# Kernel optimization log

Hardware: AMD Instinct MI355X
Metric: run time of the kernel (lower is better)

The kernel has to match this reference:

```python
import jax, jax.numpy as jnp
import numpy as np

E, DM, DH, K, DIL = 8, 512, 1024, 3, 2
N, L = 128, 128
PAD = DIL * (K - 1) // 2  # 'same' padding


def _conv1d(x, w):
    # x: [N, Cin, L], w: [Cout, Cin, K] -> [N, Cout, L]
    return jax.lax.conv_general_dilated(
        x, w, window_strides=(1,), padding=[(PAD, PAD)],
        rhs_dilation=(DIL,), dimension_numbers=("NCH", "OIH", "NCH"))


def _moe_conv(x, W, B, onehot):
    # W: [E, Cout, Cin, K], B: [E, Cout], onehot: [N, E]
    ys = jax.vmap(lambda w, b: _conv1d(x, w) + b[None, :, None])(W, B)  # [E, N, Cout, L]
    return jnp.einsum("enol,ne->nol", ys, onehot)


def setup_inputs() -> dict:
    key = jax.random.key(0)
    k1, k2, k3, k4, k5 = jax.random.split(key, 5)
    inp = jax.random.normal(k1, (N, DM, L), dtype=jnp.float32)
    # uneven per-expert sample counts summing to N (samples pre-sorted by expert)
    fwd_expert_count = jnp.asarray(np.array([10, 20, 16, 16, 12, 22, 14, 18], dtype=np.int32))
    w1 = jax.random.normal(k2, (E, DH, DM, K), dtype=jnp.float32) * 0.02
    b1 = jax.random.normal(k3, (E, DH), dtype=jnp.float32) * 0.02
    w2 = jax.random.normal(k4, (E, DM, DH, K), dtype=jnp.float32) * 0.02
    b2 = jax.random.normal(k5, (E, DM), dtype=jnp.float32) * 0.02
    return {"inp": inp, "fwd_expert_count": fwd_expert_count,
            "w1": w1, "b1": b1, "w2": w2, "b2": b2}


def reference(inp, fwd_expert_count, w1, b1, w2, b2):
    # map each sample index to its expert via cumulative counts
    cs = jnp.cumsum(fwd_expert_count)
    eid = jnp.searchsorted(cs, jnp.arange(N), side="right")  # [N]
    onehot = (eid[:, None] == jnp.arange(E)[None, :]).astype(inp.dtype)  # [N, E]
    h = _moe_conv(inp, w1, b1, onehot)       # [N, DH, L]
    h = jax.nn.gelu(h)
    out = _moe_conv(h, w2, b2, onehot)       # [N, DM, L]
    return out
```

## Files before the change

### kernel.cpp

```cpp
#include <hip/hip_runtime.h>
#include <hip/hip_bf16.h>
#include <stdint.h>


typedef __attribute__((ext_vector_type(8))) short short8;
typedef __attribute__((ext_vector_type(4))) float f32x4;

#define DMV 512
#define DHV 1024

#define OFF_X   0ull
#define OFF_H   (16ull << 20)
#define OFF_W1  (48ull << 20)
#define OFF_W2  (72ull << 20)

#define VMW(n) asm volatile("s_waitcnt vmcnt(" #n ")" ::: "memory")

__device__ __forceinline__ uint16_t f2bf(float f) {
  uint32_t u = __builtin_bit_cast(uint32_t, f);
  uint32_t r = (u + 0x7FFFu + ((u >> 16) & 1u)) >> 16;
  return (uint16_t)r;
}

__device__ __forceinline__ void async_copy16(const void* g, void* l) {
  __builtin_amdgcn_global_load_lds(
      (const __attribute__((address_space(1))) uint32_t*)g,
      (__attribute__((address_space(3))) uint32_t*)l, 16, 0, 0);
}

__device__ __forceinline__ float gelu_f(float x) {
  float u = 0.7978845608028654f * (x + 0.044715f * x * x * x);
  float t = __expf(2.0f * u);
  float th = 1.0f - 2.0f / (t + 1.0f);
  return 0.5f * x * (1.0f + th);
}

__global__ __launch_bounds__(256) void prep_x_t(const float* __restrict__ inp,
                                                uint16_t* __restrict__ xp) {
  uint32_t b = blockIdx.x;
  uint32_t s = b >> 4, cc = b & 15u;
  __shared__ uint16_t xs[32][132];
  uint32_t t = threadIdx.x;
  const float* src0 = inp + ((size_t)s * DMV + cc * 32u) * 128u;
#pragma unroll
  for (int i = 0; i < 4; ++i) {
    uint32_t idx = (uint32_t)i * 256u + t;
    uint32_t ch = idx >> 5, l4 = idx & 31u;
    float4 f = *(const float4*)(src0 + ch * 128u + l4 * 4u);
    uint2 pk;
    pk.x = (uint32_t)f2bf(f.x) | ((uint32_t)f2bf(f.y) << 16);
    pk.y = (uint32_t)f2bf(f.z) | ((uint32_t)f2bf(f.w) << 16);
    *(uint2*)&xs[ch][l4 * 4u] = pk;
  }
  __syncthreads();
  uint32_t l = t >> 1, half = t & 1u;
  uint32_t fl = ((l + 2u) >> 1) & 3u;
#pragma unroll
  for (int hi = 0; hi < 2; ++hi) {
    uint32_t sub = half * 2u + (uint32_t)hi;
    uint32_t cg = (sub ^ fl) & 3u;
    uint32_t pk[4];
#pragma unroll
    for (int p2 = 0; p2 < 4; ++p2) {
      uint32_t c0 = cg * 8u + (uint32_t)p2 * 2u;
      pk[p2] = (uint32_t)xs[c0][l] | ((uint32_t)xs[c0 + 1][l] << 16);
    }
    uint4 v; v.x = pk[0]; v.y = pk[1]; v.z = pk[2]; v.w = pk[3];
    size_t slot = (((size_t)s * 16u + cc) * 128u + l) * 4u + sub;
    *(uint4*)(xp + slot * 8u) = v;
  }
}

template <int LOGCG, int LOGO>
__global__ __launch_bounds__(256) void prep_w_c(const float* __restrict__ w,
                                                uint16_t* __restrict__ wp) {
  constexpr uint32_t C = 4u << LOGCG;
  constexpr uint32_t CCn = C >> 5;
  constexpr uint32_t MTn = 1u << (LOGO - 7);
  uint32_t t = blockIdx.x * 256u + threadIdx.x;
  uint32_t cg = t & ((1u << LOGCG) - 1u);
  uint32_t o = (t >> LOGCG) & ((1u << LOGO) - 1u);
  uint32_t e = t >> (LOGCG + LOGO);
  uint32_t row = o & 127u, mt = o >> 7;
  const float* src = w + (((size_t)(e << LOGO) + o) * C + cg * 4u) * 3u;
  float4 f0 = *(const float4*)(src);
  float4 f1 = *(const float4*)(src + 4);
  float4 f2 = *(const float4*)(src + 8);
  uint32_t cc = cg >> 3;
  uint32_t sub = ((cg >> 1) & 3u) ^ ((row >> 1) & 3u);
  uint32_t j0 = (cg & 1u) * 4u;
  size_t base = (((size_t)e * CCn + cc) * MTn + mt) * 3u;
  uint2 q;
  q.x = (uint32_t)f2bf(f0.x) | ((uint32_t)f2bf(f0.w) << 16);
  q.y = (uint32_t)f2bf(f1.z) | ((uint32_t)f2bf(f2.y) << 16);
  *(uint2*)(wp + ((base + 0u) * 128u + row) * 32u + sub * 8u + j0) = q;
  q.x = (uint32_t)f2bf(f0.y) | ((uint32_t)f2bf(f1.x) << 16);
  q.y = (uint32_t)f2bf(f1.w) | ((uint32_t)f2bf(f2.z) << 16);
  *(uint2*)(wp + ((base + 1u) * 128u + row) * 32u + sub * 8u + j0) = q;
  q.x = (uint32_t)f2bf(f0.z) | ((uint32_t)f2bf(f1.y) << 16);
  q.y = (uint32_t)f2bf(f2.x) | ((uint32_t)f2bf(f2.w) << 16);
  *(uint2*)(wp + ((base + 2u) * 128u + row) * 32u + sub * 8u + j0) = q;
}

template <int PHASE>
__global__ __launch_bounds__(256, 2) void conv_mfma(
    const uint16_t* __restrict__ bprep, const uint16_t* __restrict__ wprep,
    const float* __restrict__ bias, const int* __restrict__ cnt,
    uint16_t* __restrict__ hout, float* __restrict__ fout) {
  constexpr int CC = (PHASE == 1) ? 16 : 32;
  constexpr int MTP = (PHASE == 1) ? 8 : 4;
  constexpr int OO = (PHASE == 1) ? DHV : DMV;
  constexpr uint32_t BUFS = 24576u + 8448u;

  uint32_t b = blockIdx.x;
  constexpr uint32_t CPX = (128u * MTP) >> 3;
  uint32_t work = (b & 7u) * CPX + (b >> 3);
  const int s = work & 127;
  const int mt = work >> 7;
  int e = 0;
  {
    int cum = cnt[0];
    while (s >= cum && e < 7) { ++e; cum += cnt[e]; }
  }
  const int tid = threadIdx.x;
  const int lane = tid & 63;
  const int wv = tid >> 6;
  const int wr = wv >> 1, wc = wv & 1;
  const int l15 = lane & 15, kg = lane >> 4;

  __shared__ __align__(16) uint8_t lds[2 * BUFS];

  uint32_t aOff[4];
#pragma unroll
  for (int a = 0; a < 4; ++a) {
    uint32_t ri = (uint32_t)(wr * 64 + a * 16 + l15);
    aOff[a] = ri * 64u + (((uint32_t)kg ^ (ri >> 1)) & 3u) * 16u;
  }
  uint32_t lB[4];
#pragma unroll
  for (int bq = 0; bq < 4; ++bq) lB[bq] = (uint32_t)(wc * 64 + bq * 16 + l15);

  const uint16_t* wTile0 = wprep + ((size_t)e * CC * MTP + mt) * 12288;
  auto SA = [&](uint8_t* bw, int ccn, int k, int h) {
    async_copy16(wTile0 + (size_t)ccn * (MTP * 12288) + k * 4096 + h * 2048 + tid * 8,
                 bw + (uint32_t)k * 8192u + (uint32_t)h * 4096u + (uint32_t)tid * 16);
  };
  auto SBL = [&](uint8_t* bw, int ccn, int h) {
    async_copy16(bprep + ((size_t)s * CC + ccn) * 4096 + h * 2048 + tid * 8,
                 bw + 24576u + 128u + (uint32_t)h * 4096u + (uint32_t)tid * 16);
  };
  auto STAGE = [&](uint8_t* bw, int ccn) {
    SBL(bw, ccn, 0); SBL(bw, ccn, 1);
    SA(bw, ccn, 0, 0); SA(bw, ccn, 0, 1);
    SA(bw, ccn, 1, 0); SA(bw, ccn, 1, 1);
    SA(bw, ccn, 2, 0); SA(bw, ccn, 2, 1);
  };

  if (tid < 32) {
    uint32_t n = (uint32_t)tid >> 4, ri = ((uint32_t)tid >> 2) & 3u, sb = (uint32_t)tid & 3u;
    uint32_t rowByte = (ri < 2) ? ri * 64u : (8320u + (ri - 2) * 64u);
    uint4 z = make_uint4(0, 0, 0, 0);
    *(uint4*)(lds + n * BUFS + 24576u + rowByte + sb * 16u) = z;
  }

  STAGE(lds, 0);
  VMW(0);
  asm volatile("s_waitcnt lgkmcnt(0)" ::: "memory");
  __builtin_amdgcn_s_barrier();
  asm volatile("" ::: "memory");

  f32x4 acc[4][4] = {};

#pragma unroll 1
  for (int cc = 0; cc < CC; ++cc) {
    const uint8_t* br = lds + (uint32_t)(cc & 1) * BUFS;
    uint8_t* bw = lds + (uint32_t)((cc & 1) ^ 1) * BUFS;
    if (cc + 1 < CC) STAGE(bw, cc + 1);
#pragma unroll
    for (int k = 0; k < 3; ++k) {
      short8 af_[4], bf_[4];
#pragma unroll
      for (int q = 0; q < 4; ++q)
        af_[q] = *(const short8*)(br + aOff[q] + (uint32_t)k * 8192u);
#pragma unroll
      for (int bq = 0; bq < 4; ++bq) {
        uint32_t r_ = lB[bq] + 2u * (uint32_t)k;
        bf_[bq] = *(const short8*)(br + 24576u + r_ * 64u +
                                   (((uint32_t)kg ^ (r_ >> 1)) & 3u) * 16u);
      }
#pragma unroll
      for (int q = 0; q < 4; ++q)
#pragma unroll
        for (int bq = 0; bq < 4; ++bq)
          acc[q][bq] = __builtin_amdgcn_mfma_f32_16x16x32_bf16(
              af_[q], bf_[bq], acc[q][bq], 0, 0, 0);
    }
    if (cc + 1 < CC) {
      VMW(0);
      __builtin_amdgcn_s_barrier();
      asm volatile("" ::: "memory");
    }
  }

  if (PHASE == 1) {
#pragma unroll
    for (int a = 0; a < 4; ++a) {
      int ob = mt * 128 + wr * 64 + a * 16 + kg * 4;
      float4 bv = *(const float4*)(bias + (size_t)e * OO + ob);
      int cc2 = mt * 4 + wr * 2 + (a >> 1);
      uint32_t g = (uint32_t)((a & 1) * 2 + (kg >> 1));
      uint32_t j0 = (uint32_t)((kg & 1) * 4);
#pragma unroll
      for (int bq = 0; bq < 4; ++bq) {
        int l = wc * 64 + bq * 16 + l15;
        uint32_t flq = ((uint32_t)(l + 2) >> 1) & 3u;
        uint32_t sub = g ^ flq;
        float v0 = gelu_f(acc[a][bq][0] + bv.x);
        float v1 = gelu_f(acc[a][bq][1] + bv.y);
        float v2 = gelu_f(acc[a][bq][2] + bv.z);
        float v3 = gelu_f(acc[a][bq][3] + bv.w);
        uint2 pk;
        pk.x = (uint32_t)f2bf(v0) | ((uint32_t)f2bf(v1) << 16);
        pk.y = (uint32_t)f2bf(v2) | ((uint32_t)f2bf(v3) << 16);
        size_t ci = ((size_t)s * 32 + cc2) * 128 + l;
        *(uint2*)(hout + ci * 32 + sub * 8 + j0) = pk;
      }
    }
  } else {
#pragma unroll
    for (int a = 0; a < 4; ++a) {
      int ob = mt * 128 + wr * 64 + a * 16 + kg * 4;
      float4 bv = *(const float4*)(bias + (size_t)e * OO + ob);
      float bvr[4] = {bv.x, bv.y, bv.z, bv.w};
      float* op = fout + ((size_t)s * DMV + ob) * 128;
#pragma unroll
      for (int bq = 0; bq < 4; ++bq) {
        int l = wc * 64 + bq * 16 + l15;
#pragma unroll
        for (int r = 0; r < 4; ++r)
          op[(size_t)r * 128 + l] = acc[a][bq][r] + bvr[r];
      }
    }
  }
}

extern "C" void kernel_launch(void* const* d_in, const int* in_sizes, int n_in,
                              void* d_out, int out_size, void* d_ws, size_t ws_size,
                              hipStream_t stream) {
  const float* inp = (const float*)d_in[0];
  const int* cnt = (const int*)d_in[1];
  const float* w1 = (const float*)d_in[2];
  const float* b1 = (const float*)d_in[3];
  const float* w2 = (const float*)d_in[4];
  const float* b2 = (const float*)d_in[5];
  float* out = (float*)d_out;
  uint8_t* ws = (uint8_t*)d_ws;
  uint16_t* xp = (uint16_t*)(ws + OFF_X);
  uint16_t* hp = (uint16_t*)(ws + OFF_H);
  uint16_t* w1p = (uint16_t*)(ws + OFF_W1);
  uint16_t* w2p = (uint16_t*)(ws + OFF_W2);

  prep_x_t<<<dim3(2048), dim3(256), 0, stream>>>(inp, xp);
  prep_w_c<7, 10><<<dim3(4096), dim3(256), 0, stream>>>(w1, w1p);
  prep_w_c<8, 9><<<dim3(4096), dim3(256), 0, stream>>>(w2, w2p);
  conv_mfma<1><<<dim3(1024), dim3(256), 0, stream>>>(xp, w1p, b1, cnt, hp, nullptr);
  conv_mfma<2><<<dim3(512), dim3(256), 0, stream>>>(hp, w2p, b2, cnt, nullptr, out);
}
```

Baseline: 146.5 us.

## Load MFMA operands directly from global memory instead of LDS double-buffering

Removes the LDS staging, async global-to-LDS copies and XOR swizzle, so each lane loads its bf16 A and B fragments straight from global memory, with boundary zero-padding done by masking. The block-to-work mapping is changed to group samples per XCD, and s_setprio is raised around the MFMA bursts. The x prep buffer is moved into the output buffer to shrink workspace. This drops LDS traffic and per-stage waits, but relies on L1/L2 caching and exposes global load latency without explicit prefetching. The out-of-range B rows rely on masking after reads that may fall just before the buffer start, including reads at an offset into the output buffer.

```diff
diff --git a/kernel.cpp b/kernel.cpp
--- a/kernel.cpp
+++ b/kernel.cpp
@@ -9,23 +9,14 @@
 #define DMV 512
 #define DHV 1024
 
-#define OFF_X   0ull
-#define OFF_H   (16ull << 20)
-#define OFF_W1  (48ull << 20)
-#define OFF_W2  (72ull << 20)
-
-#define VMW(n) asm volatile("s_waitcnt vmcnt(" #n ")" ::: "memory")
+#define OFF_W1  0ull
+#define OFF_H   25165824ull
+#define OFF_W2  58720256ull
 
 __device__ __forceinline__ uint16_t f2bf(float f) {
   uint32_t u = __builtin_bit_cast(uint32_t, f);
   uint32_t r = (u + 0x7FFFu + ((u >> 16) & 1u)) >> 16;
   return (uint16_t)r;
-}
-
-__device__ __forceinline__ void async_copy16(const void* g, void* l) {
-  __builtin_amdgcn_global_load_lds(
-      (const __attribute__((address_space(1))) uint32_t*)g,
-      (__attribute__((address_space(3))) uint32_t*)l, 16, 0, 0);
 }
 
 __device__ __forceinline__ float gelu_f(float x) {
@@ -54,15 +45,13 @@
   }
   __syncthreads();
   uint32_t l = t >> 1, half = t & 1u;
-  uint32_t fl = ((l + 2u) >> 1) & 3u;
 #pragma unroll
   for (int hi = 0; hi < 2; ++hi) {
     uint32_t sub = half * 2u + (uint32_t)hi;
-    uint32_t cg = (sub ^ fl) & 3u;
     uint32_t pk[4];
 #pragma unroll
     for (int p2 = 0; p2 < 4; ++p2) {
-      uint32_t c0 = cg * 8u + (uint32_t)p2 * 2u;
+      uint32_t c0 = sub * 8u + (uint32_t)p2 * 2u;
       pk[p2] = (uint32_t)xs[c0][l] | ((uint32_t)xs[c0 + 1][l] << 16);
     }
     uint4 v; v.x = pk[0]; v.y = pk[1]; v.z = pk[2]; v.w = pk[3];
@@ -87,7 +76,7 @@
   float4 f1 = *(const float4*)(src + 4);
   float4 f2 = *(const float4*)(src + 8);
   uint32_t cc = cg >> 3;
-  uint32_t sub = ((cg >> 1) & 3u) ^ ((row >> 1) & 3u);
+  uint32_t sub = (cg >> 1) & 3u;
   uint32_t j0 = (cg & 1u) * 4u;
   size_t base = (((size_t)e * CCn + cc) * MTn + mt) * 3u;
   uint2 q;
@@ -110,96 +99,55 @@
   constexpr int CC = (PHASE == 1) ? 16 : 32;
   constexpr int MTP = (PHASE == 1) ? 8 : 4;
   constexpr int OO = (PHASE == 1) ? DHV : DMV;
-  constexpr uint32_t BUFS = 24576u + 8448u;
 
   uint32_t b = blockIdx.x;
-  constexpr uint32_t CPX = (128u * MTP) >> 3;
-  uint32_t work = (b & 7u) * CPX + (b >> 3);
-  const int s = work & 127;
-  const int mt = work >> 7;
+  uint32_t xcd = b & 7u, i = b >> 3;
+  const int s = (int)(xcd * 16u + (PHASE == 1 ? (i >> 3) : (i >> 2)));
+  const int mt = (int)(PHASE == 1 ? (i & 7u) : (i & 3u));
   int e = 0;
-  {
-    int cum = cnt[0];
-    while (s >= cum && e < 7) { ++e; cum += cnt[e]; }
-  }
+  { int cum = cnt[0]; while (s >= cum && e < 7) { ++e; cum += cnt[e]; } }
   const int tid = threadIdx.x;
   const int lane = tid & 63;
   const int wv = tid >> 6;
   const int wr = wv >> 1, wc = wv & 1;
   const int l15 = lane & 15, kg = lane >> 4;
 
-  __shared__ __align__(16) uint8_t lds[2 * BUFS];
-
-  uint32_t aOff[4];
-#pragma unroll
-  for (int a = 0; a < 4; ++a) {
-    uint32_t ri = (uint32_t)(wr * 64 + a * 16 + l15);
-    aOff[a] = ri * 64u + (((uint32_t)kg ^ (ri >> 1)) & 3u) * 16u;
-  }
-  uint32_t lB[4];
-#pragma unroll
-  for (int bq = 0; bq < 4; ++bq) lB[bq] = (uint32_t)(wc * 64 + bq * 16 + l15);
-
-  const uint16_t* wTile0 = wprep + ((size_t)e * CC * MTP + mt) * 12288;
-  auto SA = [&](uint8_t* bw, int ccn, int k, int h) {
-    async_copy16(wTile0 + (size_t)ccn * (MTP * 12288) + k * 4096 + h * 2048 + tid * 8,
-                 bw + (uint32_t)k * 8192u + (uint32_t)h * 4096u + (uint32_t)tid * 16);
-  };
-  auto SBL = [&](uint8_t* bw, int ccn, int h) {
-    async_copy16(bprep + ((size_t)s * CC + ccn) * 4096 + h * 2048 + tid * 8,
-                 bw + 24576u + 128u + (uint32_t)h * 4096u + (uint32_t)tid * 16);
-  };
-  auto STAGE = [&](uint8_t* bw, int ccn) {
-    SBL(bw, ccn, 0); SBL(bw, ccn, 1);
-    SA(bw, ccn, 0, 0); SA(bw, ccn, 0, 1);
-    SA(bw, ccn, 1, 0); SA(bw, ccn, 1, 1);
-    SA(bw, ccn, 2, 0); SA(bw, ccn, 2, 1);
-  };
-
-  if (tid < 32) {
-    uint32_t n = (uint32_t)tid >> 4, ri = ((uint32_t)tid >> 2) & 3u, sb = (uint32_t)tid & 3u;
-    uint32_t rowByte = (ri < 2) ? ri * 64u : (8320u + (ri - 2) * 64u);
-    uint4 z = make_uint4(0, 0, 0, 0);
-    *(uint4*)(lds + n * BUFS + 24576u + rowByte + sb * 16u) = z;
-  }
-
-  STAGE(lds, 0);
-  VMW(0);
-  asm volatile("s_waitcnt lgkmcnt(0)" ::: "memory");
-  __builtin_amdgcn_s_barrier();
-  asm volatile("" ::: "memory");
+  const bool mLow = (wc == 0) && (l15 < 2);
+  const bool mHigh = (wc == 1) && (l15 >= 14);
+
+  const uint16_t* aLane = wprep + ((size_t)e * CC * MTP + mt) * 12288
+                          + (uint32_t)((wr * 64 + l15) * 32 + kg * 8);
+  const uint16_t* bLane = bprep + (size_t)s * CC * 4096
+                          + (ptrdiff_t)((wc * 64 + l15 - 2) * 32 + kg * 8);
 
   f32x4 acc[4][4] = {};
+  const short8 z8 = {};
 
 #pragma unroll 1
   for (int cc = 0; cc < CC; ++cc) {
-    const uint8_t* br = lds + (uint32_t)(cc & 1) * BUFS;
-    uint8_t* bw = lds + (uint32_t)((cc & 1) ^ 1) * BUFS;
-    if (cc + 1 < CC) STAGE(bw, cc + 1);
+    const uint16_t* aP = aLane + (size_t)cc * (MTP * 12288);
+    const uint16_t* bP = bLane + (size_t)cc * 4096;
 #pragma unroll
     for (int k = 0; k < 3; ++k) {
       short8 af_[4], bf_[4];
 #pragma unroll
       for (int q = 0; q < 4; ++q)
-        af_[q] = *(const short8*)(br + aOff[q] + (uint32_t)k * 8192u);
-#pragma unroll
-      for (int bq = 0; bq < 4; ++bq) {
-        uint32_t r_ = lB[bq] + 2u * (uint32_t)k;
-        bf_[bq] = *(const short8*)(br + 24576u + r_ * 64u +
-                                   (((uint32_t)kg ^ (r_ >> 1)) & 3u) * 16u);
-      }
+        af_[q] = *(const short8*)(aP + (uint32_t)(k * 4096 + q * 512));
+#pragma unroll
+      for (int bq = 0; bq < 4; ++bq)
+        bf_[bq] = *(const short8*)(bP + (uint32_t)(k * 64 + bq * 512));
+      if (k == 0) bf_[0] = mLow ? z8 : bf_[0];
+      if (k == 2) bf_[3] = mHigh ? z8 : bf_[3];
+      __builtin_amdgcn_s_setprio(1);
 #pragma unroll
       for (int q = 0; q < 4; ++q)
 #pragma unroll
         for (int bq = 0; bq < 4; ++bq)
           acc[q][bq] = __builtin_amdgcn_mfma_f32_16x16x32_bf16(
               af_[q], bf_[bq], acc[q][bq], 0, 0, 0);
-    }
-    if (cc + 1 < CC) {
-      VMW(0);
-      __builtin_amdgcn_s_barrier();
-      asm volatile("" ::: "memory");
-    }
+      __builtin_amdgcn_s_setprio(0);
+    }
+    __builtin_amdgcn_s_barrier();
   }
 
   if (PHASE == 1) {
@@ -208,13 +156,11 @@
       int ob = mt * 128 + wr * 64 + a * 16 + kg * 4;
       float4 bv = *(const float4*)(bias + (size_t)e * OO + ob);
       int cc2 = mt * 4 + wr * 2 + (a >> 1);
-      uint32_t g = (uint32_t)((a & 1) * 2 + (kg >> 1));
+      uint32_t sub = (uint32_t)((a & 1) * 2 + (kg >> 1));
       uint32_t j0 = (uint32_t)((kg & 1) * 4);
 #pragma unroll
       for (int bq = 0; bq < 4; ++bq) {
         int l = wc * 64 + bq * 16 + l15;
-        uint32_t flq = ((uint32_t)(l + 2) >> 1) & 3u;
-        uint32_t sub = g ^ flq;
         float v0 = gelu_f(acc[a][bq][0] + bv.x);
         float v1 = gelu_f(acc[a][bq][1] + bv.y);
         float v2 = gelu_f(acc[a][bq][2] + bv.z);
@@ -255,10 +201,10 @@
   const float* b2 = (const float*)d_in[5];
   float* out = (float*)d_out;
   uint8_t* ws = (uint8_t*)d_ws;
-  uint16_t* xp = (uint16_t*)(ws + OFF_X);
+  uint16_t* w1p = (uint16_t*)(ws + OFF_W1);
   uint16_t* hp = (uint16_t*)(ws + OFF_H);
-  uint16_t* w1p = (uint16_t*)(ws + OFF_W1);
   uint16_t* w2p = (uint16_t*)(ws + OFF_W2);
+  uint16_t* xp = (uint16_t*)((uint8_t*)d_out + 4096);
 
   prep_x_t<<<dim3(2048), dim3(256), 0, stream>>>(inp, xp);
   prep_w_c<7, 10><<<dim3(4096), dim3(256), 0, stream>>>(w1, w1p);
```

Measured after the change: 225.1 us. +53.7%, slower.

## Software-pipeline LDS tap reads against MFMA with sched barriers and setprio

Applied to the files above, without the earlier changes.

Unrolls the three convolution taps by hand so that the LDS fragment reads for the next tap are issued before the MFMAs of the current tap. Scheduling barriers pin that ordering, and s_setprio raises wave priority around the MFMA groups. The B-operand swizzled LDS offsets for each tap are now precomputed outside the loop. The global-load wait moves ahead of the last tap's MFMAs, so the barrier ends each iteration. The goal is to hide LDS latency and cut address arithmetic in the inner loop, at the cost of more live registers for the double fragment sets and the precomputed offsets.

```diff
diff --git a/kernel.cpp b/kernel.cpp
--- a/kernel.cpp
+++ b/kernel.cpp
@@ -15,6 +15,7 @@
 #define OFF_W2  (72ull << 20)
 
 #define VMW(n) asm volatile("s_waitcnt vmcnt(" #n ")" ::: "memory")
+#define SB __builtin_amdgcn_sched_barrier(0)
 
 __device__ __forceinline__ uint16_t f2bf(float f) {
   uint32_t u = __builtin_bit_cast(uint32_t, f);
@@ -118,10 +119,7 @@
   const int s = work & 127;
   const int mt = work >> 7;
   int e = 0;
-  {
-    int cum = cnt[0];
-    while (s >= cum && e < 7) { ++e; cum += cnt[e]; }
-  }
+  { int cum = cnt[0]; while (s >= cum && e < 7) { ++e; cum += cnt[e]; } }
   const int tid = threadIdx.x;
   const int lane = tid & 63;
   const int wv = tid >> 6;
@@ -136,9 +134,14 @@
     uint32_t ri = (uint32_t)(wr * 64 + a * 16 + l15);
     aOff[a] = ri * 64u + (((uint32_t)kg ^ (ri >> 1)) & 3u) * 16u;
   }
-  uint32_t lB[4];
-#pragma unroll
-  for (int bq = 0; bq < 4; ++bq) lB[bq] = (uint32_t)(wc * 64 + bq * 16 + l15);
+  uint32_t bOff[3][4];
+#pragma unroll
+  for (int k = 0; k < 3; ++k)
+#pragma unroll
+    for (int bq = 0; bq < 4; ++bq) {
+      uint32_t r = (uint32_t)(wc * 64 + bq * 16 + l15 + 2 * k);
+      bOff[k][bq] = 24576u + r * 64u + (((uint32_t)kg ^ (r >> 1)) & 3u) * 16u;
+    }
 
   const uint16_t* wTile0 = wprep + ((size_t)e * CC * MTP + mt) * 12288;
   auto SA = [&](uint8_t* bw, int ccn, int k, int h) {
@@ -167,40 +170,43 @@
   VMW(0);
   asm volatile("s_waitcnt lgkmcnt(0)" ::: "memory");
   __builtin_amdgcn_s_barrier();
-  asm volatile("" ::: "memory");
 
   f32x4 acc[4][4] = {};
+
+#define READTAP(K, AF, BF)                                                     \
+  _Pragma("unroll") for (int q = 0; q < 4; ++q)                                \
+    AF[q] = *(const short8*)(br + aOff[q] + (uint32_t)(K) * 8192u);            \
+  _Pragma("unroll") for (int bq = 0; bq < 4; ++bq)                             \
+    BF[bq] = *(const short8*)(br + bOff[K][bq]);
+
+#define MFMATAP(AF, BF)                                                        \
+  __builtin_amdgcn_s_setprio(1);                                               \
+  _Pragma("unroll") for (int q = 0; q < 4; ++q)                                \
+    _Pragma("unroll") for (int bq = 0; bq < 4; ++bq)                           \
+      acc[q][bq] = __builtin_amdgcn_mfma_f32_16x16x32_bf16(                    \
+          AF[q], BF[bq], acc[q][bq], 0, 0, 0);                                 \
+  __builtin_amdgcn_s_setprio(0);
 
 #pragma unroll 1
   for (int cc = 0; cc < CC; ++cc) {
     const uint8_t* br = lds + (uint32_t)(cc & 1) * BUFS;
     uint8_t* bw = lds + (uint32_t)((cc & 1) ^ 1) * BUFS;
+    short8 a0[4], b0[4], a1[4], b1[4];
+    READTAP(0, a0, b0); SB;
     if (cc + 1 < CC) STAGE(bw, cc + 1);
-#pragma unroll
-    for (int k = 0; k < 3; ++k) {
-      short8 af_[4], bf_[4];
-#pragma unroll
-      for (int q = 0; q < 4; ++q)
-        af_[q] = *(const short8*)(br + aOff[q] + (uint32_t)k * 8192u);
-#pragma unroll
-      for (int bq = 0; bq < 4; ++bq) {
-        uint32_t r_ = lB[bq] + 2u * (uint32_t)k;
-        bf_[bq] = *(const short8*)(br + 24576u + r_ * 64u +
-                                   (((uint32_t)kg ^ (r_ >> 1)) & 3u) * 16u);
-      }
-#pragma unroll
-      for (int q = 0; q < 4; ++q)
-#pragma unroll
-        for (int bq = 0; bq < 4; ++bq)
-          acc[q][bq] = __builtin_amdgcn_mfma_f32_16x16x32_bf16(
-              af_[q], bf_[bq], acc[q][bq], 0, 0, 0);
-    }
-    if (cc + 1 < CC) {
-      VMW(0);
-      __builtin_amdgcn_s_barrier();
-      asm volatile("" ::: "memory");
-    }
-  }
+    SB;
+    READTAP(1, a1, b1); SB;
+    MFMATAP(a0, b0);
+    SB;
+    READTAP(2, a0, b0); SB;
+    MFMATAP(a1, b1);
+    SB;
+    VMW(0);
+    MFMATAP(a0, b0);
+    __builtin_amdgcn_s_barrier();
+  }
+#undef READTAP
+#undef MFMATAP
 
   if (PHASE == 1) {
 #pragma unroll
```

New measurement: 144.7 us. Within noise of the previous version (-1.2%).

## Halve conv block tile to 64 rows with 128 threads and register-cached A fragments

Applied to the files above, without the earlier changes.

The MFMA conv kernel now runs 128-thread blocks, each computing 64 output channels instead of 128, and launches twice as many blocks. The weight tile is single-buffered: A fragments for all three taps are loaded into registers before a barrier, and the next stage is then issued into the same LDS while the input tile stays double-buffered. The block-to-work mapping now groups consecutive samples per XCD, and s_setprio is placed around the MFMA bursts. This is meant to shrink LDS use for higher occupancy and better load balance, at the cost of more redundant input-tile loads and an extra barrier per chunk.

```diff
diff --git a/kernel.cpp b/kernel.cpp
--- a/kernel.cpp
+++ b/kernel.cpp
@@ -13,8 +13,6 @@
 #define OFF_H   (16ull << 20)
 #define OFF_W1  (48ull << 20)
 #define OFF_W2  (72ull << 20)
-
-#define VMW(n) asm volatile("s_waitcnt vmcnt(" #n ")" ::: "memory")
 
 __device__ __forceinline__ uint16_t f2bf(float f) {
   uint32_t u = __builtin_bit_cast(uint32_t, f);
@@ -103,111 +101,110 @@
 }
 
 template <int PHASE>
-__global__ __launch_bounds__(256, 2) void conv_mfma(
+__global__ __launch_bounds__(128, 3) void conv_mfma(
     const uint16_t* __restrict__ bprep, const uint16_t* __restrict__ wprep,
     const float* __restrict__ bias, const int* __restrict__ cnt,
     uint16_t* __restrict__ hout, float* __restrict__ fout) {
   constexpr int CC = (PHASE == 1) ? 16 : 32;
   constexpr int MTP = (PHASE == 1) ? 8 : 4;
+  constexpr int MT2 = MTP * 2;
+  constexpr int MTSH = (PHASE == 1) ? 4 : 3;
   constexpr int OO = (PHASE == 1) ? DHV : DMV;
-  constexpr uint32_t BUFS = 24576u + 8448u;
 
   uint32_t b = blockIdx.x;
-  constexpr uint32_t CPX = (128u * MTP) >> 3;
-  uint32_t work = (b & 7u) * CPX + (b >> 3);
-  const int s = work & 127;
-  const int mt = work >> 7;
+  uint32_t xcd = b & 7u, i = b >> 3;
+  const int s = (int)(xcd * 16u + (i >> MTSH));
+  const int mt = (int)(i & (MT2 - 1));
   int e = 0;
-  {
-    int cum = cnt[0];
-    while (s >= cum && e < 7) { ++e; cum += cnt[e]; }
-  }
+  { int cum = cnt[0]; while (s >= cum && e < 7) { ++e; cum += cnt[e]; } }
   const int tid = threadIdx.x;
   const int lane = tid & 63;
-  const int wv = tid >> 6;
-  const int wr = wv >> 1, wc = wv & 1;
+  const int wc = tid >> 6;
   const int l15 = lane & 15, kg = lane >> 4;
 
-  __shared__ __align__(16) uint8_t lds[2 * BUFS];
+  __shared__ __align__(16) uint8_t lds[29184];
 
   uint32_t aOff[4];
 #pragma unroll
-  for (int a = 0; a < 4; ++a) {
-    uint32_t ri = (uint32_t)(wr * 64 + a * 16 + l15);
-    aOff[a] = ri * 64u + (((uint32_t)kg ^ (ri >> 1)) & 3u) * 16u;
-  }
-  uint32_t lB[4];
-#pragma unroll
-  for (int bq = 0; bq < 4; ++bq) lB[bq] = (uint32_t)(wc * 64 + bq * 16 + l15);
-
-  const uint16_t* wTile0 = wprep + ((size_t)e * CC * MTP + mt) * 12288;
-  auto SA = [&](uint8_t* bw, int ccn, int k, int h) {
-    async_copy16(wTile0 + (size_t)ccn * (MTP * 12288) + k * 4096 + h * 2048 + tid * 8,
-                 bw + (uint32_t)k * 8192u + (uint32_t)h * 4096u + (uint32_t)tid * 16);
+  for (int q = 0; q < 4; ++q) {
+    uint32_t ri = (uint32_t)(q * 16 + l15);
+    aOff[q] = ri * 64u + (((uint32_t)kg ^ (ri >> 1)) & 3u) * 16u;
+  }
+  uint32_t bOff[3][4];
+#pragma unroll
+  for (int k = 0; k < 3; ++k)
+#pragma unroll
+    for (int bq = 0; bq < 4; ++bq) {
+      uint32_t r = (uint32_t)(wc * 64 + bq * 16 + l15 + 2 * k);
+      bOff[k][bq] = r * 64u + (((uint32_t)kg ^ (r >> 1)) & 3u) * 16u;
+    }
+
+  const uint16_t* wTile0 = wprep + ((size_t)e * CC * MTP + (mt >> 1)) * 12288
+                           + (uint32_t)(mt & 1) * 2048;
+  const uint16_t* xBase = bprep + (size_t)s * CC * 4096;
+
+  auto SA = [&](int ccn, int k, int h) {
+    async_copy16(wTile0 + (size_t)ccn * (MTP * 12288) + k * 4096 + h * 1024 + tid * 8,
+                 lds + (uint32_t)(k * 4096 + h * 2048) + (uint32_t)tid * 16);
   };
-  auto SBL = [&](uint8_t* bw, int ccn, int h) {
-    async_copy16(bprep + ((size_t)s * CC + ccn) * 4096 + h * 2048 + tid * 8,
-                 bw + 24576u + 128u + (uint32_t)h * 4096u + (uint32_t)tid * 16);
+  auto SBL = [&](int buf, int ccn, int h) {
+    async_copy16(xBase + (size_t)ccn * 4096 + h * 1024 + tid * 8,
+                 lds + 12288u + (uint32_t)buf * 8448u + 128u +
+                     (uint32_t)h * 2048u + (uint32_t)tid * 16);
   };
-  auto STAGE = [&](uint8_t* bw, int ccn) {
-    SBL(bw, ccn, 0); SBL(bw, ccn, 1);
-    SA(bw, ccn, 0, 0); SA(bw, ccn, 0, 1);
-    SA(bw, ccn, 1, 0); SA(bw, ccn, 1, 1);
-    SA(bw, ccn, 2, 0); SA(bw, ccn, 2, 1);
+  auto STAGE = [&](int buf, int ccn) {
+    SA(ccn, 0, 0); SA(ccn, 0, 1); SA(ccn, 1, 0);
+    SA(ccn, 1, 1); SA(ccn, 2, 0); SA(ccn, 2, 1);
+    SBL(buf, ccn, 0); SBL(buf, ccn, 1); SBL(buf, ccn, 2); SBL(buf, ccn, 3);
   };
 
   if (tid < 32) {
     uint32_t n = (uint32_t)tid >> 4, ri = ((uint32_t)tid >> 2) & 3u, sb = (uint32_t)tid & 3u;
     uint32_t rowByte = (ri < 2) ? ri * 64u : (8320u + (ri - 2) * 64u);
     uint4 z = make_uint4(0, 0, 0, 0);
-    *(uint4*)(lds + n * BUFS + 24576u + rowByte + sb * 16u) = z;
-  }
-
-  STAGE(lds, 0);
-  VMW(0);
-  asm volatile("s_waitcnt lgkmcnt(0)" ::: "memory");
-  __builtin_amdgcn_s_barrier();
-  asm volatile("" ::: "memory");
+    *(uint4*)(lds + 12288u + n * 8448u + rowByte + sb * 16u) = z;
+  }
+
+  STAGE(0, 0);
+  __syncthreads();
 
   f32x4 acc[4][4] = {};
 
 #pragma unroll 1
   for (int cc = 0; cc < CC; ++cc) {
-    const uint8_t* br = lds + (uint32_t)(cc & 1) * BUFS;
-    uint8_t* bw = lds + (uint32_t)((cc & 1) ^ 1) * BUFS;
-    if (cc + 1 < CC) STAGE(bw, cc + 1);
+    const uint8_t* bb = lds + 12288u + (uint32_t)(cc & 1) * 8448u;
+    short8 afr[3][4];
+#pragma unroll
+    for (int k = 0; k < 3; ++k)
+#pragma unroll
+      for (int q = 0; q < 4; ++q)
+        afr[k][q] = *(const short8*)(lds + (uint32_t)(k * 4096) + aOff[q]);
+    __syncthreads();
+    if (cc + 1 < CC) STAGE((cc + 1) & 1, cc + 1);
 #pragma unroll
     for (int k = 0; k < 3; ++k) {
-      short8 af_[4], bf_[4];
-#pragma unroll
-      for (int q = 0; q < 4; ++q)
-        af_[q] = *(const short8*)(br + aOff[q] + (uint32_t)k * 8192u);
-#pragma unroll
-      for (int bq = 0; bq < 4; ++bq) {
-        uint32_t r_ = lB[bq] + 2u * (uint32_t)k;
-        bf_[bq] = *(const short8*)(br + 24576u + r_ * 64u +
-                                   (((uint32_t)kg ^ (r_ >> 1)) & 3u) * 16u);
-      }
+      short8 bf[4];
+#pragma unroll
+      for (int bq = 0; bq < 4; ++bq)
+        bf[bq] = *(const short8*)(bb + bOff[k][bq]);
+      __builtin_amdgcn_s_setprio(1);
 #pragma unroll
       for (int q = 0; q < 4; ++q)
 #pragma unroll
         for (int bq = 0; bq < 4; ++bq)
           acc[q][bq] = __builtin_amdgcn_mfma_f32_16x16x32_bf16(
-              af_[q], bf_[bq], acc[q][bq], 0, 0, 0);
-    }
-    if (cc + 1 < CC) {
-      VMW(0);
-      __builtin_amdgcn_s_barrier();
-      asm volatile("" ::: "memory");
-    }
+              afr[k][q], bf[bq], acc[q][bq], 0, 0, 0);
+      __builtin_amdgcn_s_setprio(0);
+    }
+    if (cc + 1 < CC) __syncthreads();
   }
 
   if (PHASE == 1) {
 #pragma unroll
     for (int a = 0; a < 4; ++a) {
-      int ob = mt * 128 + wr * 64 + a * 16 + kg * 4;
+      int ob = mt * 64 + a * 16 + kg * 4;
       float4 bv = *(const float4*)(bias + (size_t)e * OO + ob);
-      int cc2 = mt * 4 + wr * 2 + (a >> 1);
+      int cc2 = mt * 2 + (a >> 1);
       uint32_t g = (uint32_t)((a & 1) * 2 + (kg >> 1));
       uint32_t j0 = (uint32_t)((kg & 1) * 4);
 #pragma unroll
@@ -229,7 +226,7 @@
   } else {
 #pragma unroll
     for (int a = 0; a < 4; ++a) {
-      int ob = mt * 128 + wr * 64 + a * 16 + kg * 4;
+      int ob = mt * 64 + a * 16 + kg * 4;
       float4 bv = *(const float4*)(bias + (size_t)e * OO + ob);
       float bvr[4] = {bv.x, bv.y, bv.z, bv.w};
       float* op = fout + ((size_t)s * DMV + ob) * 128;
@@ -263,6 +260,6 @@
   prep_x_t<<<dim3(2048), dim3(256), 0, stream>>>(inp, xp);
   prep_w_c<7, 10><<<dim3(4096), dim3(256), 0, stream>>>(w1, w1p);
   prep_w_c<8, 9><<<dim3(4096), dim3(256), 0, stream>>>(w2, w2p);
-  conv_mfma<1><<<dim3(1024), dim3(256), 0, stream>>>(xp, w1p, b1, cnt, hp, nullptr);
-  conv_mfma<2><<<dim3(512), dim3(256), 0, stream>>>(hp, w2p, b2, cnt, nullptr, out);
-}
+  conv_mfma<1><<<dim3(2048), dim3(128), 0, stream>>>(xp, w1p, b1, cnt, hp, nullptr);
+  conv_mfma<2><<<dim3(1024), dim3(128), 0, stream>>>(hp, w2p, b2, cnt, nullptr, out);
+}
```

Result: slower. 158.8 us (+8.4%).
